# Performance work log

Measured on AMD Instinct MI355X. Metric: run time of the kernel, lower is better.

## Reference

```python
import jax, jax.numpy as jnp
import numpy as np
from jax import lax

# Conv config (mirrors Conv2dMem init_kwargs)
B, CIN, H, W = 16, 256, 56, 56
COUT, K = 256, 3
STRIDE, PAD = 1, 1
INPUT_BW = 8   # sum(input_slice [1,1,2,4])
WEIGHT_BW = 8  # sum(weight_slice [1,1,2,4])
IN_GRAN = (1, 32)    # input_quant_gran
W_GRAN = (32, 32)    # weight_quant_gran
H_OUT = (H + 2 * PAD - K) // STRIDE + 1
W_OUT = (W + 2 * PAD - K) // STRIDE + 1


def block_fake_quant(x, gran, bw):
    """Per-block symmetric fake quantization to `bw` bits (1 sign bit).

    Blocks of size gran=(gr, gc) over the last two dims share one max-abs scale.
    Bit-slicing then exactly recombines to this quantized integer, so the
    ideal (noise-free) MapReduceDot math equals this quant-dequant + GEMM.
    """
    gr, gc = gran
    lead = x.shape[:-2]
    R, C = x.shape[-2], x.shape[-1]
    xb = x.reshape(*lead, R // gr, gr, C // gc, gc)
    m = jnp.max(jnp.abs(xb), axis=(-3, -1), keepdims=True)
    levels = 2.0 ** (bw - 1) - 1.0
    scale = jnp.where(m > 0, m / levels, jnp.ones_like(m))
    xq = jnp.round(xb / scale) * scale
    return xq.reshape(x.shape)


def setup_inputs() -> dict:
    key = jax.random.key(0)
    kx, kw, kb = jax.random.split(key, 3)
    x = jax.random.normal(kx, (B, CIN, H, W), dtype=jnp.float32)
    fan_in = CIN * K * K
    # kaiming_uniform(a=sqrt(5)) -> U(-1/sqrt(fan_in), 1/sqrt(fan_in))
    bound = 1.0 / np.sqrt(fan_in)
    weight = jax.random.uniform(kw, (COUT, CIN, K, K), dtype=jnp.float32,
                                minval=-bound, maxval=bound)
    bias = jax.random.uniform(kb, (COUT,), dtype=jnp.float32,
                              minval=-bound, maxval=bound)
    return {"x": x, "weight": weight, "bias": bias}


def reference(x, weight, bias):
    # Unfold: (B, CIN*K*K, H_OUT*W_OUT) with torch-compatible (c, kh, kw) feature order
    patches = lax.conv_general_dilated_patches(
        x, filter_shape=(K, K), window_strides=(STRIDE, STRIDE),
        padding=((PAD, PAD), (PAD, PAD)))
    L = H_OUT * W_OUT
    cdim = CIN * K * K
    inp_unf = patches.reshape(B, cdim, L).transpose(0, 2, 1)  # (B, L, cdim)
    # Per-block quantize input (gran (1,32) over (L, cdim)) and weight (gran (32,32))
    xq = block_fake_quant(inp_unf, IN_GRAN, INPUT_BW)
    wmat = weight.reshape(COUT, cdim).T  # (cdim, COUT)
    wq = block_fake_quant(wmat, W_GRAN, WEIGHT_BW)
    out = jnp.einsum('blc,co->blo', xq, wq) + bias  # (B, L, COUT)
    # fold with 1x1 kernel == reshape back to image layout
    return out.transpose(0, 2, 1).reshape(B, COUT, H_OUT, W_OUT)
```

## Files before the change

kernel.cpp:

```cpp
#include <hip/hip_runtime.h>

typedef unsigned short u16;
typedef unsigned int u32;
typedef __bf16 bf16x8 __attribute__((ext_vector_type(8)));
typedef float f32x4 __attribute__((ext_vector_type(4)));
typedef u32 u32x4 __attribute__((ext_vector_type(4)));

#define CIN 256
#define COUT_ 256
#define HW 56
#define LIMG 3136
#define CDIM 2304
#define NK 36

static __device__ __forceinline__ u16 f32_bf16(float f) {
    u32 u = __float_as_uint(f);
    u += 0x7fffu + ((u >> 16) & 1u);
    return (u16)(u >> 16);
}

__global__ void quant_w_kernel(const float* __restrict__ w, u16* __restrict__ wq) {
    const int kb = blockIdx.x % 72;
    const int ob = blockIdx.x / 72;
    const int k0 = kb * 32, o0 = ob * 32;
    const int t = threadIdx.x;
    float v[16];
    float mx = 0.f;
#pragma unroll
    for (int i = 0; i < 16; ++i) {
        const int e = i * 64 + t;
        const int oo = e >> 5, cc = e & 31;
        const float val = w[(o0 + oo) * CDIM + k0 + cc];
        v[i] = val;
        mx = fmaxf(mx, fabsf(val));
    }
#pragma unroll
    for (int d = 1; d < 64; d <<= 1) mx = fmaxf(mx, __shfl_xor(mx, d, 64));
    const float scale = mx > 0.f ? mx * (1.f / 127.f) : 1.f;
    const float inv   = mx > 0.f ? 127.f / mx : 1.f;
#pragma unroll
    for (int i = 0; i < 16; ++i) {
        const int e = i * 64 + t;
        const int oo = e >> 5, cc = e & 31;
        const int o = o0 + oo, k = k0 + cc;
        const float q = rintf(v[i] * inv) * scale;
        wq[o * CDIM + (k ^ ((o & 7) << 3))] = f32_bf16(q);
    }
}

__global__ __launch_bounds__(256, 3)
void conv_gemm_kernel(const float* __restrict__ x, const u16* __restrict__ wq,
                      const float* __restrict__ bias, float* __restrict__ out) {
    __shared__ __align__(16) u16 Bs[256 * 64];
    __shared__ __align__(16) u16 As[64 * 64];
    __shared__ float smax[256];

    const int tid = threadIdx.x;
    const int lane = tid & 63;
    const int q = __builtin_amdgcn_readfirstlane(tid >> 6);
    const int wm = q & 1, wn = q >> 1;

    const int m0 = blockIdx.x * 64;
    const int img = m0 / LIMG;
    const int l0 = m0 - img * LIMG;

    const int l = l0 + lane;
    const int oh = l / HW, ow = l - oh * HW;
    u32 pb = 0;
#pragma unroll
    for (int p = 0; p < 9; ++p) {
        const int kh = p / 3, kw = p - (p / 3) * 3;
        const int ih = oh + kh - 1, iw = ow + kw - 1;
        const u32 ok = (ih >= 0 && ih < HW && iw >= 0 && iw < HW) ? 1u : 0u;
        pb |= ok << p;
    }
    const float* __restrict__ xim = x + (size_t)img * (CIN * LIMG);

    f32x4 acc[2][8];
#pragma unroll
    for (int m = 0; m < 2; ++m)
#pragma unroll
        for (int n = 0; n < 8; ++n)
            acc[m][n] = (f32x4){0.f, 0.f, 0.f, 0.f};

    float valsA[16], valsB[16];

    auto gather_issue = [&](float (&vals)[16], int t) {
#pragma unroll
        for (int j = 0; j < 16; ++j) {
            const int f = t * 64 + (q << 4) + j;
            const int c = f / 9;
            const int r9 = f - c * 9;
            const int kh = r9 / 3;
            const int kw = r9 - kh * 3;
            const int dsp = (kh - 1) * HW + (kw - 1);
            int e = l + dsp;
            e = min(max(e, 0), LIMG - 1);
            vals[j] = xim[(u32)(c * LIMG + e)];
        }
    };

    auto step = [&](int t, float (&vC)[16], float (&vN)[16], bool last) {
#pragma unroll
        for (int i = 0; i < 8; ++i) {
            const int colt = i * 32 + (tid >> 3);
            const u16* g = wq + (size_t)colt * CDIM + t * 64 + (tid & 7) * 8;
            u16* lp = &Bs[0] + i * 2048 + tid * 8;
            __builtin_amdgcn_global_load_lds(
                (const __attribute__((address_space(1))) void*)g,
                (__attribute__((address_space(3))) void*)lp, 16, 0, 0);
        }
        asm volatile("" ::: "memory");
        __builtin_amdgcn_sched_barrier(0);

        if (!last) gather_issue(vN, t + 1);

        float vm[16];
        float mx = 0.f;
#pragma unroll
        for (int j = 0; j < 16; ++j) {
            const int f = t * 64 + (q << 4) + j;
            const int c = f / 9;
            const int r9 = f - c * 9;
            const u32 bit = (pb >> r9) & 1u;
            const float v = __uint_as_float(__float_as_uint(vC[j]) & (0u - bit));
            vm[j] = v;
            mx = fmaxf(mx, fabsf(v));
        }
        smax[tid] = mx;
        asm volatile("s_waitcnt lgkmcnt(0)" ::: "memory");
        __builtin_amdgcn_sched_barrier(0);
        __builtin_amdgcn_s_barrier();
        __builtin_amdgcn_sched_barrier(0);

        const float pm = smax[tid ^ 64];
        const float m2 = fmaxf(mx, pm);
        const float inv = m2 > 0.f ? __builtin_amdgcn_rcpf(m2) * 127.f : 0.f;
        const float scale = m2 * (1.f / 127.f);
        union { u16 h[16]; u32x4 v4[2]; } pk;
#pragma unroll
        for (int j = 0; j < 16; ++j) {
            const float r = rintf(vm[j] * inv);
            pk.h[j] = f32_bf16(r * scale);
        }
        {
            const int s0 = q * 2;
            *(u32x4*)&As[lane * 64 + (((s0    ) ^ (lane & 7)) << 3)] = pk.v4[0];
            *(u32x4*)&As[lane * 64 + (((s0 + 1) ^ (lane & 7)) << 3)] = pk.v4[1];
        }
        if (!last) { asm volatile("s_waitcnt lgkmcnt(0) vmcnt(16)" ::: "memory"); }
        else       { asm volatile("s_waitcnt lgkmcnt(0) vmcnt(0)"  ::: "memory"); }
        __builtin_amdgcn_sched_barrier(0);
        __builtin_amdgcn_s_barrier();
        __builtin_amdgcn_sched_barrier(0);

        const int arow = wm * 32 + (lane & 15);
#pragma unroll
        for (int kk = 0; kk < 2; ++kk) {
            const int s = kk * 4 + (lane >> 4);
            const bf16x8 a0 = *(const bf16x8*)&As[(arow     ) * 64 + ((s ^ ((arow     ) & 7)) << 3)];
            const bf16x8 a1 = *(const bf16x8*)&As[(arow + 16) * 64 + ((s ^ ((arow + 16) & 7)) << 3)];
#pragma unroll
            for (int n = 0; n < 8; ++n) {
                const int col = wn * 128 + n * 16 + (lane & 15);
                const bf16x8 b = *(const bf16x8*)&Bs[col * 64 + ((s ^ (col & 7)) << 3)];
                acc[0][n] = __builtin_amdgcn_mfma_f32_16x16x32_bf16(a0, b, acc[0][n], 0, 0, 0);
                acc[1][n] = __builtin_amdgcn_mfma_f32_16x16x32_bf16(a1, b, acc[1][n], 0, 0, 0);
            }
        }
        __builtin_amdgcn_sched_barrier(0);
        __builtin_amdgcn_s_barrier();
        __builtin_amdgcn_sched_barrier(0);
    };

    gather_issue(valsA, 0);

#pragma unroll 1
    for (int p = 0; p < 17; ++p) {
        step(2 * p,     valsA, valsB, false);
        step(2 * p + 1, valsB, valsA, false);
    }
    step(34, valsA, valsB, false);
    step(35, valsB, valsA, true);

#pragma unroll
    for (int n = 0; n < 8; ++n) {
        const int col = wn * 128 + n * 16 + (lane & 15);
        const float bz = bias[col];
#pragma unroll
        for (int m = 0; m < 2; ++m) {
            f32x4 a = acc[m][n];
            a[0] += bz; a[1] += bz; a[2] += bz; a[3] += bz;
            const int row = wm * 32 + m * 16 + ((lane >> 4) << 2);
            const size_t idx = ((size_t)(img * COUT_ + col)) * LIMG + l0 + row;
            *(f32x4*)(out + idx) = a;
        }
    }
}

extern "C" void kernel_launch(void* const* d_in, const int* in_sizes, int n_in,
                              void* d_out, int out_size, void* d_ws, size_t ws_size,
                              hipStream_t stream) {
    const float* x    = (const float*)d_in[0];
    const float* w    = (const float*)d_in[1];
    const float* bias = (const float*)d_in[2];
    float* out = (float*)d_out;
    u16* wq = (u16*)d_ws;

    quant_w_kernel<<<576, 64, 0, stream>>>(w, wq);
    conv_gemm_kernel<<<784, 256, 0, stream>>>(x, wq, bias, out);
}
```

Baseline: 264.9 us.

## Double GEMM M-tile to 128 rows and keep per-row quant scale in-thread

Result: no change. 259.7 us (-1.9%).

```diff
diff --git a/kernel.cpp b/kernel.cpp
--- a/kernel.cpp
+++ b/kernel.cpp
@@ -11,7 +11,8 @@
 #define HW 56
 #define LIMG 3136
 #define CDIM 2304
-#define NK 36
+#define NSTEP 36
+#define NTILE 392
 
 static __device__ __forceinline__ u16 f32_bf16(float f) {
     u32 u = __float_as_uint(f);
@@ -48,24 +49,28 @@
     }
 }
 
-__global__ __launch_bounds__(256, 3)
+__global__ __launch_bounds__(256, 2)
 void conv_gemm_kernel(const float* __restrict__ x, const u16* __restrict__ wq,
                       const float* __restrict__ bias, float* __restrict__ out) {
     __shared__ __align__(16) u16 Bs[256 * 64];
-    __shared__ __align__(16) u16 As[64 * 64];
-    __shared__ float smax[256];
-
-    const int tid = threadIdx.x;
+    __shared__ __align__(16) u16 As[128 * 64];
+
+    const int tid  = threadIdx.x;
     const int lane = tid & 63;
-    const int q = __builtin_amdgcn_readfirstlane(tid >> 6);
-    const int wm = q & 1, wn = q >> 1;
-
-    const int m0 = blockIdx.x * 64;
-    const int img = m0 / LIMG;
-    const int l0 = m0 - img * LIMG;
-
-    const int l = l0 + lane;
-    const int oh = l / HW, ow = l - oh * HW;
+    const int wid  = __builtin_amdgcn_readfirstlane(tid >> 6);
+    const int wm   = wid & 1;
+    const int wn   = wid >> 1;
+    const int h    = wn;
+
+    const int tile = (blockIdx.x & 7) * 49 + (blockIdx.x >> 3);
+    const int m0   = tile * 128;
+
+    const int r = wm * 64 + lane;
+    const int m = m0 + r;
+    const int img = m / 3136;
+    const int l   = m - img * 3136;
+    const int oh  = l / HW, ow = l - (l / HW) * HW;
+
     u32 pb = 0;
 #pragma unroll
     for (int p = 0; p < 9; ++p) {
@@ -76,31 +81,33 @@
     }
     const float* __restrict__ xim = x + (size_t)img * (CIN * LIMG);
 
-    f32x4 acc[2][8];
-#pragma unroll
-    for (int m = 0; m < 2; ++m)
+    f32x4 acc[4][8];
+#pragma unroll
+    for (int mi = 0; mi < 4; ++mi)
 #pragma unroll
         for (int n = 0; n < 8; ++n)
-            acc[m][n] = (f32x4){0.f, 0.f, 0.f, 0.f};
-
-    float valsA[16], valsB[16];
-
-    auto gather_issue = [&](float (&vals)[16], int t) {
-#pragma unroll
-        for (int j = 0; j < 16; ++j) {
-            const int f = t * 64 + (q << 4) + j;
-            const int c = f / 9;
-            const int r9 = f - c * 9;
-            const int kh = r9 / 3;
-            const int kw = r9 - kh * 3;
-            const int dsp = (kh - 1) * HW + (kw - 1);
+            acc[mi][n] = (f32x4){0.f, 0.f, 0.f, 0.f};
+
+    float va[32];
+
+    auto gather_issue = [&](int t) {
+#pragma unroll
+        for (int j = 0; j < 32; ++j) {
+            const int k = t * 64 + h * 32 + j;
+            const int c = k / 9;
+            const int p = k - c * 9;
+            const int kh = p / 3;
+            const int dsp = (kh - 1) * HW + (p - kh * 3) - 1;
             int e = l + dsp;
             e = min(max(e, 0), LIMG - 1);
-            vals[j] = xim[(u32)(c * LIMG + e)];
+            va[j] = xim[(u32)(c * LIMG + e)];
         }
     };
 
-    auto step = [&](int t, float (&vC)[16], float (&vN)[16], bool last) {
+    gather_issue(0);
+
+#pragma unroll 1
+    for (int t = 0; t < NSTEP; ++t) {
 #pragma unroll
         for (int i = 0; i < 8; ++i) {
             const int colt = i * 32 + (tid >> 3);
@@ -113,87 +120,101 @@
         asm volatile("" ::: "memory");
         __builtin_amdgcn_sched_barrier(0);
 
-        if (!last) gather_issue(vN, t + 1);
-
-        float vm[16];
-        float mx = 0.f;
-#pragma unroll
-        for (int j = 0; j < 16; ++j) {
-            const int f = t * 64 + (q << 4) + j;
-            const int c = f / 9;
-            const int r9 = f - c * 9;
-            const u32 bit = (pb >> r9) & 1u;
-            const float v = __uint_as_float(__float_as_uint(vC[j]) & (0u - bit));
-            vm[j] = v;
-            mx = fmaxf(mx, fabsf(v));
-        }
-        smax[tid] = mx;
-        asm volatile("s_waitcnt lgkmcnt(0)" ::: "memory");
+#pragma unroll
+        for (int j = 0; j < 32; ++j) {
+            const int k = t * 64 + h * 32 + j;
+            const int c = k / 9;
+            const int p = k - c * 9;
+            const u32 bit = (pb >> p) & 1u;
+            va[j] = __uint_as_float(__float_as_uint(va[j]) & (0u - bit));
+        }
+        float t16[16];
+#pragma unroll
+        for (int j = 0; j < 16; ++j) t16[j] = fmaxf(fabsf(va[j]), fabsf(va[j + 16]));
+#pragma unroll
+        for (int j = 0; j < 8; ++j) t16[j] = fmaxf(t16[j], t16[j + 8]);
+#pragma unroll
+        for (int j = 0; j < 4; ++j) t16[j] = fmaxf(t16[j], t16[j + 4]);
+        const float mx = fmaxf(fmaxf(t16[0], t16[1]), fmaxf(t16[2], t16[3]));
+
+        const float inv   = mx > 0.f ? 127.f * __builtin_amdgcn_rcpf(mx) : 0.f;
+        const float scale = mx * (1.f / 127.f);
+
+        union { u16 hh[32]; u32x4 v4[4]; } pk;
+#pragma unroll
+        for (int j = 0; j < 32; ++j)
+            pk.hh[j] = f32_bf16(rintf(va[j] * inv) * scale);
+#pragma unroll
+        for (int w = 0; w < 4; ++w) {
+            const int s = h * 4 + w;
+            *(u32x4*)&As[r * 64 + ((s ^ (r & 7)) << 3)] = pk.v4[w];
+        }
+        asm volatile("" ::: "memory");
+        __builtin_amdgcn_sched_barrier(0);
+
+        if (t < NSTEP - 1) {
+            gather_issue(t + 1);
+            asm volatile("s_waitcnt lgkmcnt(0) vmcnt(32)" ::: "memory");
+        } else {
+            asm volatile("s_waitcnt lgkmcnt(0) vmcnt(0)" ::: "memory");
+        }
         __builtin_amdgcn_sched_barrier(0);
         __builtin_amdgcn_s_barrier();
-        __builtin_amdgcn_sched_barrier(0);
-
-        const float pm = smax[tid ^ 64];
-        const float m2 = fmaxf(mx, pm);
-        const float inv = m2 > 0.f ? __builtin_amdgcn_rcpf(m2) * 127.f : 0.f;
-        const float scale = m2 * (1.f / 127.f);
-        union { u16 h[16]; u32x4 v4[2]; } pk;
-#pragma unroll
-        for (int j = 0; j < 16; ++j) {
-            const float r = rintf(vm[j] * inv);
-            pk.h[j] = f32_bf16(r * scale);
-        }
-        {
-            const int s0 = q * 2;
-            *(u32x4*)&As[lane * 64 + (((s0    ) ^ (lane & 7)) << 3)] = pk.v4[0];
-            *(u32x4*)&As[lane * 64 + (((s0 + 1) ^ (lane & 7)) << 3)] = pk.v4[1];
-        }
-        if (!last) { asm volatile("s_waitcnt lgkmcnt(0) vmcnt(16)" ::: "memory"); }
-        else       { asm volatile("s_waitcnt lgkmcnt(0) vmcnt(0)"  ::: "memory"); }
+        asm volatile("" ::: "memory");
+        __builtin_amdgcn_sched_barrier(0);
+
+        const int arow_b = wm * 64 + (lane & 15);
+        const int bcol_b = wn * 128 + (lane & 15);
+        const int sl = lane >> 4;
+#pragma unroll
+        for (int kk = 0; kk < 2; ++kk) {
+            const int s = kk * 4 + sl;
+            bf16x8 a[4];
+#pragma unroll
+            for (int mi = 0; mi < 4; ++mi) {
+                const int ar = arow_b + mi * 16;
+                a[mi] = *(const bf16x8*)&As[ar * 64 + ((s ^ (ar & 7)) << 3)];
+            }
+#pragma unroll
+            for (int n = 0; n < 8; ++n) {
+                const int col = bcol_b + n * 16;
+                const bf16x8 b = *(const bf16x8*)&Bs[col * 64 + ((s ^ (col & 7)) << 3)];
+#pragma unroll
+                for (int mi = 0; mi < 4; ++mi)
+                    acc[mi][n] = __builtin_amdgcn_mfma_f32_16x16x32_bf16(a[mi], b, acc[mi][n], 0, 0, 0);
+            }
+        }
+        asm volatile("" ::: "memory");
         __builtin_amdgcn_sched_barrier(0);
         __builtin_amdgcn_s_barrier();
-        __builtin_amdgcn_sched_barrier(0);
-
-        const int arow = wm * 32 + (lane & 15);
-#pragma unroll
-        for (int kk = 0; kk < 2; ++kk) {
-            const int s = kk * 4 + (lane >> 4);
-            const bf16x8 a0 = *(const bf16x8*)&As[(arow     ) * 64 + ((s ^ ((arow     ) & 7)) << 3)];
-            const bf16x8 a1 = *(const bf16x8*)&As[(arow + 16) * 64 + ((s ^ ((arow + 16) & 7)) << 3)];
-#pragma unroll
-            for (int n = 0; n < 8; ++n) {
-                const int col = wn * 128 + n * 16 + (lane & 15);
-                const bf16x8 b = *(const bf16x8*)&Bs[col * 64 + ((s ^ (col & 7)) << 3)];
-                acc[0][n] = __builtin_amdgcn_mfma_f32_16x16x32_bf16(a0, b, acc[0][n], 0, 0, 0);
-                acc[1][n] = __builtin_amdgcn_mfma_f32_16x16x32_bf16(a1, b, acc[1][n], 0, 0, 0);
-            }
-        }
-        __builtin_amdgcn_sched_barrier(0);
-        __builtin_amdgcn_s_barrier();
-        __builtin_amdgcn_sched_barrier(0);
-    };
-
-    gather_issue(valsA, 0);
-
-#pragma unroll 1
-    for (int p = 0; p < 17; ++p) {
-        step(2 * p,     valsA, valsB, false);
-        step(2 * p + 1, valsB, valsA, false);
-    }
-    step(34, valsA, valsB, false);
-    step(35, valsB, valsA, true);
-
+        asm volatile("" ::: "memory");
+        __builtin_amdgcn_sched_barrier(0);
+    }
+
+    const int si    = __builtin_amdgcn_readfirstlane(m0 / 3136);
+    const int l0    = m0 - si * 3136;
+    const bool split = l0 > 3136 - 128;
+    const int rb = wm * 64 + ((lane >> 4) << 2);
 #pragma unroll
     for (int n = 0; n < 8; ++n) {
         const int col = wn * 128 + n * 16 + (lane & 15);
         const float bz = bias[col];
 #pragma unroll
-        for (int m = 0; m < 2; ++m) {
-            f32x4 a = acc[m][n];
+        for (int mi = 0; mi < 4; ++mi) {
+            f32x4 a = acc[mi][n];
             a[0] += bz; a[1] += bz; a[2] += bz; a[3] += bz;
-            const int row = wm * 32 + m * 16 + ((lane >> 4) << 2);
-            const size_t idx = ((size_t)(img * COUT_ + col)) * LIMG + l0 + row;
-            *(f32x4*)(out + idx) = a;
+            const int row = rb + mi * 16;
+            if (!split) {
+                *(f32x4*)&out[((size_t)(si * COUT_ + col)) * LIMG + l0 + row] = a;
+            } else {
+#pragma unroll
+                for (int j = 0; j < 4; ++j) {
+                    const int mm = m0 + row + j;
+                    const int ig = mm / 3136;
+                    const int ll = mm - ig * 3136;
+                    out[((size_t)(ig * COUT_ + col)) * LIMG + ll] = a[j];
+                }
+            }
         }
     }
 }
@@ -208,5 +229,5 @@
     u16* wq = (u16*)d_ws;
 
     quant_w_kernel<<<576, 64, 0, stream>>>(w, wq);
-    conv_gemm_kernel<<<784, 256, 0, stream>>>(x, wq, bias, out);
-}
+    conv_gemm_kernel<<<NTILE, 256, 0, stream>>>(x, wq, bias, out);
+}
```
